# Kernel optimization log

Measured on AMD Instinct MI355X. Metric: run time of the kernel, lower is better.

Reference implementation:

```python
import jax, jax.numpy as jnp
import numpy as np

H = 128          # h_dim
N_NODES = 100000
N_EDGES = 1600000
N_GRAPHS = 256
EPS_BN = 1e-5


def setup_inputs() -> dict:
    key = jax.random.key(0)
    ks = jax.random.split(key, 12)
    x = jax.random.normal(ks[0], (N_NODES, 4), dtype=jnp.float32)
    edge_index = jax.random.randint(ks[1], (2, N_EDGES), 0, N_NODES, dtype=jnp.int64)
    batch = jnp.sort(jax.random.randint(ks[2], (N_NODES,), 0, N_GRAPHS, dtype=jnp.int64))
    # Linear weights (xavier-ish scale), stored as [in, out]
    W1 = jax.random.normal(ks[3], (4, H), dtype=jnp.float32) * (1.0 / np.sqrt(4))
    W2 = jax.random.normal(ks[4], (H, H), dtype=jnp.float32) * (1.0 / np.sqrt(H))
    W3 = jax.random.normal(ks[5], (H, H), dtype=jnp.float32) * (1.0 / np.sqrt(H))
    Wfc = jax.random.normal(ks[6], (H, 1), dtype=jnp.float32) * (1.0 / np.sqrt(H))
    def bn_params(k):
        k1, k2, k3, k4 = jax.random.split(k, 4)
        gamma = 1.0 + 0.1 * jax.random.normal(k1, (H,), dtype=jnp.float32)
        beta = 0.1 * jax.random.normal(k2, (H,), dtype=jnp.float32)
        mean = 0.1 * jax.random.normal(k3, (H,), dtype=jnp.float32)
        var = 1.0 + 0.1 * jax.random.uniform(k4, (H,), dtype=jnp.float32)
        return gamma, beta, mean, var
    g1, b1, m1, v1 = bn_params(ks[7])
    g2, b2, m2, v2 = bn_params(ks[8])
    g3, b3, m3, v3 = bn_params(ks[9])
    return {
        "x": x, "edge_index": edge_index, "batch": batch,
        "W1": W1, "g1": g1, "b1": b1, "m1": m1, "v1": v1,
        "W2": W2, "g2": g2, "b2": b2, "m2": m2, "v2": v2,
        "W3": W3, "g3": g3, "b3": b3, "m3": m3, "v3": v3,
        "Wfc": Wfc,
    }


def _gin_layer(h, src, dst, W, gamma, beta, mean, var):
    # GINConv with eps=0: mlp(x + sum_{j in N(i)} x_j)
    aggr = jax.ops.segment_sum(h[src], dst, num_segments=N_NODES)
    z = (h + aggr) @ W                                  # Linear(bias=False)
    z = (z - mean) * (gamma / jnp.sqrt(var + EPS_BN)) + beta  # BatchNorm1d (eval)
    return jax.nn.relu(z)


def reference(x, edge_index, batch,
              W1, g1, b1, m1, v1,
              W2, g2, b2, m2, v2,
              W3, g3, b3, m3, v3,
              Wfc):
    src, dst = edge_index[0], edge_index[1]
    h = _gin_layer(x, src, dst, W1, g1, b1, m1, v1)
    h = _gin_layer(h, src, dst, W2, g2, b2, m2, v2)
    h = _gin_layer(h, src, dst, W3, g3, b3, m3, v3)
    # dropout: identity in eval mode
    sums = jax.ops.segment_sum(h, batch, num_segments=N_GRAPHS)      # [G, H]
    cnts = jax.ops.segment_sum(jnp.ones((N_NODES, 1), h.dtype), batch,
                               num_segments=N_GRAPHS)                # [G, 1]
    pooled = sums / jnp.maximum(cnts, 1.0)
    return jax.nn.sigmoid(pooled @ Wfc)                               # [G, 1]
```

## Files before the change

### kernel.cpp

```cpp
#include <hip/hip_runtime.h>
#include <hip/hip_fp8.h>
#include <math.h>

#define N_NODES 100000
#define N_EDGES 1600000
#define N_GRAPHS 256
#define H 128
#define EPS_BN 1e-5f
#define ELLW 64

#define PSZ 256
#define PSH 8
#define P_PART 391
#define NB_BLD 782
#define EPT_B 8
#define EPB_B (256 * EPT_B)

typedef unsigned int uint;
typedef unsigned short ushort;
typedef __attribute__((ext_vector_type(8))) short bf16x8;
typedef __attribute__((ext_vector_type(4))) float f32x4;
typedef __attribute__((ext_vector_type(2))) float f32x2;
typedef __attribute__((ext_vector_type(4))) int i32x4;

__device__ __forceinline__ uint f2bf_bits(float x) {
    uint u = __float_as_uint(x);
    return (u + 0x7fffu + ((u >> 16) & 1u)) >> 16;
}
__device__ __forceinline__ uint pack_bf2(float a, float b) {
    return f2bf_bits(a) | (f2bf_bits(b) << 16);
}

__device__ __forceinline__ unsigned char f32_to_fp8(float x) {
#if __has_builtin(__builtin_amdgcn_cvt_pk_fp8_f32)
    int v = __builtin_amdgcn_cvt_pk_fp8_f32(x, 0.0f, 0, false);
    return (unsigned char)(v & 0xff);
#else
    __hip_fp8_e4m3 q(x);
    return (unsigned char)q.__x;
#endif
}
__device__ __forceinline__ f32x4 fp8x4_to_f32x4(uint v) {
    f32x4 r;
#if __has_builtin(__builtin_amdgcn_cvt_pk_f32_fp8)
    f32x2 lo = __builtin_amdgcn_cvt_pk_f32_fp8((int)v, false);
    f32x2 hi = __builtin_amdgcn_cvt_pk_f32_fp8((int)v, true);
    r.x = lo.x; r.y = lo.y; r.z = hi.x; r.w = hi.y;
#else
    __hip_fp8_e4m3 a, b, c, d;
    a.__x = (unsigned char)(v & 0xff);
    b.__x = (unsigned char)((v >> 8) & 0xff);
    c.__x = (unsigned char)((v >> 16) & 0xff);
    d.__x = (unsigned char)((v >> 24) & 0xff);
    r.x = (float)a; r.y = (float)b; r.z = (float)c; r.w = (float)d;
#endif
    return r;
}

__global__ __launch_bounds__(256) void k_hist(const int* __restrict__ dst,
                                              int* __restrict__ hist,
                                              const int* __restrict__ batch,
                                              int* __restrict__ gstart,
                                              const float* __restrict__ W2,
                                              ushort* __restrict__ Wpk2,
                                              const float* __restrict__ W3,
                                              ushort* __restrict__ Wpk3,
                                              float* __restrict__ Gz,
                                              uint* __restrict__ Hf8pad) {
    __shared__ int h[P_PART];
    int b = blockIdx.x;
    if (b < NB_BLD) {
        for (int i = threadIdx.x; i < P_PART; i += 256) h[i] = 0;
        __syncthreads();
        int base = b * EPB_B + threadIdx.x * EPT_B;
        #pragma unroll
        for (int j = 0; j < EPT_B / 4; j++) {
            int e = base + j * 4;
            if (e + 4 <= N_EDGES) {
                i32x4 d = __builtin_nontemporal_load((const i32x4*)&dst[e]);
                atomicAdd(&h[d.x >> PSH], 1);
                atomicAdd(&h[d.y >> PSH], 1);
                atomicAdd(&h[d.z >> PSH], 1);
                atomicAdd(&h[d.w >> PSH], 1);
            }
        }
        __syncthreads();
        for (int i = threadIdx.x; i < P_PART; i += 256)
            hist[b * P_PART + i] = h[i];
        return;
    }
    if (b < 1174) {
        int n = (b - NB_BLD) * 256 + threadIdx.x;
        if (n >= N_NODES) return;
        int g = batch[n];
        int gp = (n == 0) ? -1 : batch[n - 1];
        for (int gr = gp + 1; gr <= g; gr++) gstart[gr] = n;
        if (n == N_NODES - 1) {
            for (int gr = g + 1; gr <= N_GRAPHS; gr++) gstart[gr] = N_NODES;
        }
        return;
    }
    if (b >= 1190) {
        if (threadIdx.x < N_GRAPHS) Gz[threadIdx.x] = 0.0f;
        if (threadIdx.x < 32) Hf8pad[threadIdx.x] = 0u;
        return;
    }
    const float* W = (b < 1182) ? W2 : W3;
    ushort* Wpk = (b < 1182) ? Wpk2 : Wpk3;
    int t = ((b < 1182) ? (b - 1174) : (b - 1182)) * 256 + threadIdx.x;
    int lane = t & 63, nt = (t >> 6) & 7, kt = t >> 9;
    int n = nt * 16 + (lane & 15);
    int kbase = kt * 32 + (lane >> 4) * 8;
    ushort v[8];
    #pragma unroll
    for (int j = 0; j < 8; j++)
        v[j] = (ushort)f2bf_bits(W[(size_t)(kbase + j) * H + n]);
    uint4 pk;
    pk.x = (uint)v[0] | ((uint)v[1] << 16);
    pk.y = (uint)v[2] | ((uint)v[3] << 16);
    pk.z = (uint)v[4] | ((uint)v[5] << 16);
    pk.w = (uint)v[6] | ((uint)v[7] << 16);
    *(uint4*)&Wpk[(size_t)t * 8] = pk;
}

__global__ __launch_bounds__(256) void k_scan_a(const int* __restrict__ hist,
                                                int* __restrict__ offs,
                                                int* __restrict__ tot) {
    __shared__ int lds[256];
    int p = blockIdx.x;
    int t = threadIdx.x;
    int v0 = 0, v1 = 0, v2 = 0, v3 = 0;
    int b0 = t * 4;
    if (b0 + 0 < NB_BLD) v0 = hist[(b0 + 0) * P_PART + p];
    if (b0 + 1 < NB_BLD) v1 = hist[(b0 + 1) * P_PART + p];
    if (b0 + 2 < NB_BLD) v2 = hist[(b0 + 2) * P_PART + p];
    if (b0 + 3 < NB_BLD) v3 = hist[(b0 + 3) * P_PART + p];
    int tt = v0 + v1 + v2 + v3;
    lds[t] = tt;
    __syncthreads();
    for (int off = 1; off < 256; off <<= 1) {
        int tmp = (t >= off) ? lds[t - off] : 0;
        __syncthreads();
        lds[t] += tmp;
        __syncthreads();
    }
    int run = lds[t] - tt;
    if (b0 + 0 < NB_BLD) { offs[(b0 + 0) * P_PART + p] = run; run += v0; }
    if (b0 + 1 < NB_BLD) { offs[(b0 + 1) * P_PART + p] = run; run += v1; }
    if (b0 + 2 < NB_BLD) { offs[(b0 + 2) * P_PART + p] = run; run += v2; }
    if (b0 + 3 < NB_BLD) { offs[(b0 + 3) * P_PART + p] = run; run += v3; }
    if (t == 255) tot[p] = lds[255];
}

__global__ void k_scan_b(const int* __restrict__ tot, int* __restrict__ parr) {
    __shared__ int lds[512];
    int p = threadIdx.x;
    int v = (p < P_PART) ? tot[p] : 0;
    lds[p] = v;
    __syncthreads();
    for (int off = 1; off < 512; off <<= 1) {
        int tmp = (p >= off) ? lds[p - off] : 0;
        __syncthreads();
        lds[p] += tmp;
        __syncthreads();
    }
    if (p < P_PART) parr[p] = lds[p] - v;
    if (p == 0) parr[P_PART] = N_EDGES;
}

__global__ __launch_bounds__(256) void k_scatter(const int* __restrict__ src,
                                                 const int* __restrict__ dst,
                                                 const int* __restrict__ offs,
                                                 const int* __restrict__ parr,
                                                 uint* __restrict__ ebuf) {
    __shared__ int lofs[P_PART];
    for (int i = threadIdx.x; i < P_PART; i += 256)
        lofs[i] = offs[blockIdx.x * P_PART + i] + parr[i];
    __syncthreads();
    int base = blockIdx.x * EPB_B + threadIdx.x * EPT_B;
    #pragma unroll
    for (int j = 0; j < EPT_B / 4; j++) {
        int e = base + j * 4;
        if (e + 4 <= N_EDGES) {
            i32x4 d = __builtin_nontemporal_load((const i32x4*)&dst[e]);
            i32x4 s = __builtin_nontemporal_load((const i32x4*)&src[e]);
            #pragma unroll
            for (int k = 0; k < 4; k++) {
                int dk = (k == 0) ? d.x : (k == 1) ? d.y : (k == 2) ? d.z : d.w;
                int sk = (k == 0) ? s.x : (k == 1) ? s.y : (k == 2) ? s.z : s.w;
                int pos = atomicAdd(&lofs[dk >> PSH], 1);
                ebuf[pos] = ((uint)sk << 8) | ((uint)dk & 255u);
            }
        }
    }
}

__global__ __launch_bounds__(256) void k_build(const uint* __restrict__ ebuf,
                                               const int* __restrict__ parr,
                                               int* __restrict__ cnt,
                                               int* __restrict__ ell) {
    __shared__ int lc[PSZ];
    int p = blockIdx.x;
    for (int i = threadIdx.x; i < PSZ; i += 256) lc[i] = 0;
    __syncthreads();
    int e0 = parr[p], e1 = parr[p + 1];
    int nb = p * PSZ;
    for (int i = e0 + threadIdx.x; i < e1; i += 256) {
        uint sd = ebuf[i];
        int dl = (int)(sd & 255u);
        int slot = atomicAdd(&lc[dl], 1);
        if (slot < ELLW) ell[(size_t)(nb + dl) * ELLW + slot] = (int)(sd >> 8);
    }
    __syncthreads();
    for (int i = threadIdx.x; i < PSZ; i += 256) {
        int n = nb + i;
        if (n < N_NODES) {
            int c = lc[i];
            cnt[n] = c;
            int cc = (c < ELLW) ? c : ELLW;
            int cp = (cc + 15) & ~15;
            if (cp > ELLW) cp = ELLW;
            for (int slot = cc; slot < cp; slot++)
                ell[(size_t)n * ELLW + slot] = N_NODES;
        }
    }
}

__global__ __launch_bounds__(256) void k_layer1(
    const float* __restrict__ x, const int* __restrict__ cnt,
    const int* __restrict__ ell, const float* __restrict__ W1,
    const float* __restrict__ gamma, const float* __restrict__ beta,
    const float* __restrict__ mean, const float* __restrict__ var,
    uint* __restrict__ Hf8) {
    __shared__ float scs[128], shs[128];
    int tid = threadIdx.x;
    if (tid < 128) {
        float sc = gamma[tid] * rsqrtf(var[tid] + EPS_BN);
        scs[tid] = sc;
        shs[tid] = beta[tid] - mean[tid] * sc;
    }
    __syncthreads();
    int lane = tid & 63, wave = tid >> 6;
    int sub = lane >> 4, m = lane & 15;
    int n = blockIdx.x * 16 + wave * 4 + sub;
    if (n >= N_NODES) return;
    int cn = cnt[n]; if (cn > ELLW) cn = ELLW;
    const int* row = &ell[(size_t)n * ELLW];
    const char* xb = (const char*)x;
    float4 acc = {0.f, 0.f, 0.f, 0.f};
    for (int e = m; e < cn; e += 16) {
        float4 v = *(const float4*)(xb + ((uint)row[e] << 4));
        acc.x += v.x; acc.y += v.y; acc.z += v.z; acc.w += v.w;
    }
    #pragma unroll
    for (int off = 8; off > 0; off >>= 1) {
        acc.x += __shfl_down(acc.x, off, 16);
        acc.y += __shfl_down(acc.y, off, 16);
        acc.z += __shfl_down(acc.z, off, 16);
        acc.w += __shfl_down(acc.w, off, 16);
    }
    int src = lane & 48;
    float4 xs = *(const float4*)(xb + ((uint)n << 4));
    float uu[4];
    uu[0] = __shfl(acc.x, src, 64) + xs.x;
    uu[1] = __shfl(acc.y, src, 64) + xs.y;
    uu[2] = __shfl(acc.z, src, 64) + xs.z;
    uu[3] = __shfl(acc.w, src, 64) + xs.w;
    int j0 = m * 8;
    float z[8] = {0.f, 0.f, 0.f, 0.f, 0.f, 0.f, 0.f, 0.f};
    #pragma unroll
    for (int k = 0; k < 4; k++) {
        float4 wa = *(const float4*)&W1[k * H + j0];
        float4 wb = *(const float4*)&W1[k * H + j0 + 4];
        z[0] += uu[k] * wa.x; z[1] += uu[k] * wa.y;
        z[2] += uu[k] * wa.z; z[3] += uu[k] * wa.w;
        z[4] += uu[k] * wb.x; z[5] += uu[k] * wb.y;
        z[6] += uu[k] * wb.z; z[7] += uu[k] * wb.w;
    }
    #pragma unroll
    for (int i = 0; i < 8; i++)
        z[i] = fmaxf(z[i] * scs[j0 + i] + shs[j0 + i], 0.0f);
    uint2 q;
    q.x = (uint)f32_to_fp8(z[0]) | ((uint)f32_to_fp8(z[1]) << 8)
        | ((uint)f32_to_fp8(z[2]) << 16) | ((uint)f32_to_fp8(z[3]) << 24);
    q.y = (uint)f32_to_fp8(z[4]) | ((uint)f32_to_fp8(z[5]) << 8)
        | ((uint)f32_to_fp8(z[6]) << 16) | ((uint)f32_to_fp8(z[7]) << 24);
    *(uint2*)&Hf8[(size_t)n * 32 + m * 2] = q;
}

__global__ __launch_bounds__(256) void k_aggr128(
    const uint* __restrict__ Hf8, const int* __restrict__ cnt,
    const int* __restrict__ ell, uint* __restrict__ Ubf) {
    int t = blockIdx.x * 256 + threadIdx.x;
    int n = t >> 6, lane = t & 63;
    if (n >= N_NODES) return;
    int g = lane >> 4, c8 = lane & 15;
    const int* row = &ell[(size_t)n * ELLW];
    const char* Hb = (const char*)Hf8;
    uint co = (uint)c8 << 3;
    i32x4 id = *(const i32x4*)(row + 4 * g);
    uint2 sp = {0u, 0u};
    if (g == 0) sp = *(const uint2*)(Hb + (((uint)n << 7) | co));
    int cn = cnt[n]; if (cn > ELLW) cn = ELLW;
    int cnp = (cn + 15) & ~15; if (cnp > ELLW) cnp = ELLW;

    f32x4 A = {0.f, 0.f, 0.f, 0.f};
    f32x4 B = {0.f, 0.f, 0.f, 0.f};
    for (int e = 0; e < cnp; e += 16) {
        i32x4 idn = id;
        if (e + 16 < cnp) idn = *(const i32x4*)(row + e + 16 + 4 * g);
        uint2 p0 = *(const uint2*)(Hb + (((uint)id.x << 7) | co));
        uint2 p1 = *(const uint2*)(Hb + (((uint)id.y << 7) | co));
        uint2 p2 = *(const uint2*)(Hb + (((uint)id.z << 7) | co));
        uint2 p3 = *(const uint2*)(Hb + (((uint)id.w << 7) | co));
        f32x4 l0 = fp8x4_to_f32x4(p0.x), h0 = fp8x4_to_f32x4(p0.y);
        f32x4 l1 = fp8x4_to_f32x4(p1.x), h1 = fp8x4_to_f32x4(p1.y);
        f32x4 l2 = fp8x4_to_f32x4(p2.x), h2 = fp8x4_to_f32x4(p2.y);
        f32x4 l3 = fp8x4_to_f32x4(p3.x), h3 = fp8x4_to_f32x4(p3.y);
        A += (l0 + l1) + (l2 + l3);
        B += (h0 + h1) + (h2 + h3);
        id = idn;
    }
    if (g == 0) {
        A += fp8x4_to_f32x4(sp.x);
        B += fp8x4_to_f32x4(sp.y);
    }
    #pragma unroll
    for (int off = 32; off >= 16; off >>= 1) {
        A.x += __shfl_down(A.x, off, 64);
        A.y += __shfl_down(A.y, off, 64);
        A.z += __shfl_down(A.z, off, 64);
        A.w += __shfl_down(A.w, off, 64);
        B.x += __shfl_down(B.x, off, 64);
        B.y += __shfl_down(B.y, off, 64);
        B.z += __shfl_down(B.z, off, 64);
        B.w += __shfl_down(B.w, off, 64);
    }
    if (g == 0) {
        uint4 ov;
        ov.x = pack_bf2(A.x, A.y);
        ov.y = pack_bf2(A.z, A.w);
        ov.z = pack_bf2(B.x, B.y);
        ov.w = pack_bf2(B.z, B.w);
        *(uint4*)&Ubf[(size_t)n * 64 + c8 * 4] = ov;
    }
}

__global__ __launch_bounds__(256) void k_gemm_mfma(
    const uint* __restrict__ Ubf, const uint* __restrict__ Wpk,
    const float* __restrict__ gamma, const float* __restrict__ beta,
    const float* __restrict__ mean, const float* __restrict__ var,
    unsigned char* __restrict__ Hf8,
    const int* __restrict__ batch, const float* __restrict__ Wfc,
    float* __restrict__ Gz, int mode) {
    __shared__ uint lds_u[64 * 68];
    __shared__ float sc_s[128], sh_s[128];
    __shared__ float wfc[128];
    __shared__ int bb[64];
    __shared__ float sblk[64];
    int tid = threadIdx.x;
    int row0 = blockIdx.x * 64;
    if (tid < 128) {
        float sc = gamma[tid] * rsqrtf(var[tid] + EPS_BN);
        sc_s[tid] = sc;
        sh_s[tid] = beta[tid] - mean[tid] * sc;
    }
    if (mode == 2) {
        if (tid < 128) wfc[tid] = Wfc[tid];
        if (tid < 64) {
            int rr = row0 + tid;
            bb[tid] = (rr < N_NODES) ? batch[rr] : -1;
        }
    }
    #pragma unroll
    for (int it = 0; it < 4; it++) {
        int r = it * 16 + (tid >> 4);
        int c = (tid & 15) * 4;
        int gr = row0 + r; if (gr >= N_NODES) gr = N_NODES - 1;
        uint4 v = *(const uint4*)&Ubf[(size_t)gr * 64 + c];
        *(uint4*)&lds_u[r * 68 + c] = v;
    }
    __syncthreads();

    int wave = tid >> 6, lane = tid & 63;
    int m = lane & 15, quad = lane >> 4;
    bf16x8 a[4];
    #pragma unroll
    for (int kt = 0; kt < 4; kt++)
        a[kt] = *(const bf16x8*)&lds_u[(wave * 16 + m) * 68 + kt * 16 + quad * 4];

    f32x4 acc[8];
    #pragma unroll
    for (int nt = 0; nt < 8; nt++) acc[nt] = (f32x4){0.f, 0.f, 0.f, 0.f};

    #pragma unroll
    for (int nt = 0; nt < 8; nt++) {
        #pragma unroll
        for (int kt = 0; kt < 4; kt++) {
            bf16x8 b = *(const bf16x8*)&Wpk[((size_t)(kt * 8 + nt) * 64 + lane) * 4];
            acc[nt] = __builtin_amdgcn_mfma_f32_16x16x32_bf16(a[kt], b, acc[nt], 0, 0, 0);
        }
    }

    if (mode == 1) {
        #pragma unroll
        for (int nt = 0; nt < 8; nt++) {
            int col = nt * 16 + m;
            float sc = sc_s[col], sh = sh_s[col];
            #pragma unroll
            for (int r = 0; r < 4; r++) {
                int row = row0 + wave * 16 + quad * 4 + r;
                if (row < N_NODES) {
                    float z = fmaxf(acc[nt][r] * sc + sh, 0.0f);
                    Hf8[(size_t)row * 128 + col] = f32_to_fp8(z);
                }
            }
        }
    } else {
        float pr[4] = {0.f, 0.f, 0.f, 0.f};
        #pragma unroll
        for (int nt = 0; nt < 8; nt++) {
            int col = nt * 16 + m;
            float sc = sc_s[col], sh = sh_s[col];
            float wf = wfc[col];
            #pragma unroll
            for (int r = 0; r < 4; r++) {
                float z = fmaxf(acc[nt][r] * sc + sh, 0.0f);
                pr[r] += z * wf;
            }
        }
        #pragma unroll
        for (int r = 0; r < 4; r++) {
            float p = pr[r];
            p += __shfl_down(p, 8, 16);
            p += __shfl_down(p, 4, 16);
            p += __shfl_down(p, 2, 16);
            p += __shfl_down(p, 1, 16);
            if (m == 0) sblk[wave * 16 + quad * 4 + r] = p;
        }
        __syncthreads();
        if (tid == 0) {
            int i = 0;
            while (i < 64 && row0 + i < N_NODES) {
                int g = bb[i];
                float s = 0.0f;
                while (i < 64 && row0 + i < N_NODES && bb[i] == g) {
                    s += sblk[i]; i++;
                }
                atomicAdd(&Gz[g], s);
            }
        }
    }
}

__global__ void k_fc(const float* __restrict__ Gz, const int* __restrict__ gstart,
                     float* __restrict__ out) {
    int g = threadIdx.x;
    if (g < N_GRAPHS) {
        int c = gstart[g + 1] - gstart[g];
        float z = Gz[g] / fmaxf((float)c, 1.0f);
        out[g] = 1.0f / (1.0f + expf(-z));
    }
}

extern "C" void kernel_launch(void* const* d_in, const int* in_sizes, int n_in,
                              void* d_out, int out_size, void* d_ws, size_t ws_size,
                              hipStream_t stream) {
    const float* x     = (const float*)d_in[0];
    const int*   ei    = (const int*)d_in[1];
    const int*   batch = (const int*)d_in[2];
    const float* W1    = (const float*)d_in[3];
    const float* g1    = (const float*)d_in[4];
    const float* b1    = (const float*)d_in[5];
    const float* m1    = (const float*)d_in[6];
    const float* v1    = (const float*)d_in[7];
    const float* W2    = (const float*)d_in[8];
    const float* g2    = (const float*)d_in[9];
    const float* b2    = (const float*)d_in[10];
    const float* m2    = (const float*)d_in[11];
    const float* v2    = (const float*)d_in[12];
    const float* W3    = (const float*)d_in[13];
    const float* g3    = (const float*)d_in[14];
    const float* b3    = (const float*)d_in[15];
    const float* m3    = (const float*)d_in[16];
    const float* v3    = (const float*)d_in[17];
    const float* Wfc   = (const float*)d_in[18];
    float* out = (float*)d_out;

    const int* srcp = ei;
    const int* dstp = ei + N_EDGES;

    uint* Ubf  = (uint*)d_ws;
    uint* Hf8u = Ubf + (size_t)N_NODES * 64;
    int* cnt   = (int*)(Hf8u + (size_t)N_NODES * 32 + 32);
    int* ell   = cnt + N_NODES;
    int* gstart = ell + (size_t)N_NODES * ELLW;
    ushort* Wpk2 = (ushort*)(gstart + 260);
    ushort* Wpk3 = Wpk2 + 16384;
    int* hist  = (int*)(Wpk3 + 16384);
    int* offs  = hist + NB_BLD * P_PART;
    int* parr  = offs + NB_BLD * P_PART;
    int* tot   = parr + 400;
    float* Gz  = (float*)(tot + 400);
    uint* ebuf = Ubf;
    uint* Hf8pad = Hf8u + (size_t)N_NODES * 32;

    k_hist<<<1191, 256, 0, stream>>>(dstp, hist, batch, gstart, W2, Wpk2, W3, Wpk3,
                                     Gz, Hf8pad);
    k_scan_a<<<P_PART, 256, 0, stream>>>(hist, offs, tot);
    k_scan_b<<<1, 512, 0, stream>>>(tot, parr);
    k_scatter<<<NB_BLD, 256, 0, stream>>>(srcp, dstp, offs, parr, ebuf);
    k_build<<<P_PART, 256, 0, stream>>>(ebuf, parr, cnt, ell);

    k_layer1<<<(N_NODES + 15) / 16, 256, 0, stream>>>(
        x, cnt, ell, W1, g1, b1, m1, v1, Hf8u);
    k_aggr128<<<(N_NODES * 64 + 255) / 256, 256, 0, stream>>>(Hf8u, cnt, ell, Ubf);
    k_gemm_mfma<<<(N_NODES + 63) / 64, 256, 0, stream>>>(
        Ubf, (const uint*)Wpk2, g2, b2, m2, v2, (unsigned char*)Hf8u,
        batch, Wfc, Gz, 1);
    k_aggr128<<<(N_NODES * 64 + 255) / 256, 256, 0, stream>>>(Hf8u, cnt, ell, Ubf);
    k_gemm_mfma<<<(N_NODES + 63) / 64, 256, 0, stream>>>(
        Ubf, (const uint*)Wpk3, g3, b3, m3, v3, (unsigned char*)Hf8u,
        batch, Wfc, Gz, 2);
    k_fc<<<1, 256, 0, stream>>>(Gz, gstart, out);
}
```

Before: 271.6 us.

## Fold partition scan and final FC into neighboring kernels; coalesce fp8 stores

Removes the single-block scan kernel by having each scatter and build block recompute the partition prefix sum of tot in shared memory. Removes the final FC kernel by having the last-finishing block of the layer-3 gemm compute the mean and sigmoid, detected with an atomic counter and a fence. In layer 2, the fp8 activations are staged through shared memory and written as 16-byte row chunks instead of byte-wise stores. The cost is redundant per-block scans and an extra barrier and atomic in the gemm.

```diff
diff --git a/kernel.cpp b/kernel.cpp
--- a/kernel.cpp
+++ b/kernel.cpp
@@ -57,6 +57,27 @@
     return r;
 }
 
+__device__ __forceinline__ void scan_parr(const int* __restrict__ tot,
+                                          int* lparr, int* ltmp) {
+    int t = threadIdx.x;
+    int i0 = 2 * t, i1 = 2 * t + 1;
+    int a = (i0 < P_PART) ? tot[i0] : 0;
+    int b = (i1 < P_PART) ? tot[i1] : 0;
+    int s = a + b;
+    ltmp[t] = s;
+    __syncthreads();
+    for (int off = 1; off < 256; off <<= 1) {
+        int v = (t >= off) ? ltmp[t - off] : 0;
+        __syncthreads();
+        ltmp[t] += v;
+        __syncthreads();
+    }
+    int ex = ltmp[t] - s;
+    if (i0 < 392) lparr[i0] = ex;
+    if (i1 < 392) lparr[i1] = ex + a;
+    __syncthreads();
+}
+
 __global__ __launch_bounds__(256) void k_hist(const int* __restrict__ dst,
                                               int* __restrict__ hist,
                                               const int* __restrict__ batch,
@@ -66,7 +87,8 @@
                                               const float* __restrict__ W3,
                                               ushort* __restrict__ Wpk3,
                                               float* __restrict__ Gz,
-                                              uint* __restrict__ Hf8pad) {
+                                              uint* __restrict__ Hf8pad,
+                                              int* __restrict__ done) {
     __shared__ int h[P_PART];
     int b = blockIdx.x;
     if (b < NB_BLD) {
@@ -103,6 +125,7 @@
     if (b >= 1190) {
         if (threadIdx.x < N_GRAPHS) Gz[threadIdx.x] = 0.0f;
         if (threadIdx.x < 32) Hf8pad[threadIdx.x] = 0u;
+        if (threadIdx.x == 0) *done = 0;
         return;
     }
     const float* W = (b < 1182) ? W2 : W3;
@@ -152,30 +175,17 @@
     if (t == 255) tot[p] = lds[255];
 }
 
-__global__ void k_scan_b(const int* __restrict__ tot, int* __restrict__ parr) {
-    __shared__ int lds[512];
-    int p = threadIdx.x;
-    int v = (p < P_PART) ? tot[p] : 0;
-    lds[p] = v;
-    __syncthreads();
-    for (int off = 1; off < 512; off <<= 1) {
-        int tmp = (p >= off) ? lds[p - off] : 0;
-        __syncthreads();
-        lds[p] += tmp;
-        __syncthreads();
-    }
-    if (p < P_PART) parr[p] = lds[p] - v;
-    if (p == 0) parr[P_PART] = N_EDGES;
-}
-
 __global__ __launch_bounds__(256) void k_scatter(const int* __restrict__ src,
                                                  const int* __restrict__ dst,
                                                  const int* __restrict__ offs,
-                                                 const int* __restrict__ parr,
+                                                 const int* __restrict__ tot,
                                                  uint* __restrict__ ebuf) {
     __shared__ int lofs[P_PART];
+    __shared__ int ltmp[256];
+    __shared__ int lparr[392];
+    scan_parr(tot, lparr, ltmp);
     for (int i = threadIdx.x; i < P_PART; i += 256)
-        lofs[i] = offs[blockIdx.x * P_PART + i] + parr[i];
+        lofs[i] = offs[blockIdx.x * P_PART + i] + lparr[i];
     __syncthreads();
     int base = blockIdx.x * EPB_B + threadIdx.x * EPT_B;
     #pragma unroll
@@ -196,14 +206,17 @@
 }
 
 __global__ __launch_bounds__(256) void k_build(const uint* __restrict__ ebuf,
-                                               const int* __restrict__ parr,
+                                               const int* __restrict__ tot,
                                                int* __restrict__ cnt,
                                                int* __restrict__ ell) {
     __shared__ int lc[PSZ];
+    __shared__ int ltmp[256];
+    __shared__ int lparr[392];
+    scan_parr(tot, lparr, ltmp);
     int p = blockIdx.x;
     for (int i = threadIdx.x; i < PSZ; i += 256) lc[i] = 0;
     __syncthreads();
-    int e0 = parr[p], e1 = parr[p + 1];
+    int e0 = lparr[p], e1 = lparr[p + 1];
     int nb = p * PSZ;
     for (int i = e0 + threadIdx.x; i < e1; i += 256) {
         uint sd = ebuf[i];
@@ -352,12 +365,15 @@
     const float* __restrict__ mean, const float* __restrict__ var,
     unsigned char* __restrict__ Hf8,
     const int* __restrict__ batch, const float* __restrict__ Wfc,
-    float* __restrict__ Gz, int mode) {
+    float* __restrict__ Gz, const int* __restrict__ gstart,
+    float* __restrict__ out, int* __restrict__ done, int mode) {
     __shared__ uint lds_u[64 * 68];
     __shared__ float sc_s[128], sh_s[128];
     __shared__ float wfc[128];
     __shared__ int bb[64];
     __shared__ float sblk[64];
+    __shared__ int lastblk;
+    unsigned char* lds_o = (unsigned char*)lds_u;
     int tid = threadIdx.x;
     int row0 = blockIdx.x * 64;
     if (tid < 128) {
@@ -388,6 +404,7 @@
     #pragma unroll
     for (int kt = 0; kt < 4; kt++)
         a[kt] = *(const bf16x8*)&lds_u[(wave * 16 + m) * 68 + kt * 16 + quad * 4];
+    __syncthreads();
 
     f32x4 acc[8];
     #pragma unroll
@@ -409,12 +426,19 @@
             float sc = sc_s[col], sh = sh_s[col];
             #pragma unroll
             for (int r = 0; r < 4; r++) {
-                int row = row0 + wave * 16 + quad * 4 + r;
-                if (row < N_NODES) {
-                    float z = fmaxf(acc[nt][r] * sc + sh, 0.0f);
-                    Hf8[(size_t)row * 128 + col] = f32_to_fp8(z);
-                }
+                int rl = wave * 16 + quad * 4 + r;
+                float z = fmaxf(acc[nt][r] * sc + sh, 0.0f);
+                lds_o[rl * 128 + col] = f32_to_fp8(z);
             }
+        }
+        __syncthreads();
+        #pragma unroll
+        for (int i = tid; i < 512; i += 256) {
+            int r = i >> 3;
+            int off = (i & 7) * 16;
+            int grow = row0 + r;
+            if (grow < N_NODES)
+                *(uint4*)&Hf8[(size_t)grow * 128 + off] = *(const uint4*)&lds_o[i * 16];
         }
     } else {
         float pr[4] = {0.f, 0.f, 0.f, 0.f};
@@ -449,17 +473,16 @@
                 }
                 atomicAdd(&Gz[g], s);
             }
-        }
-    }
-}
-
-__global__ void k_fc(const float* __restrict__ Gz, const int* __restrict__ gstart,
-                     float* __restrict__ out) {
-    int g = threadIdx.x;
-    if (g < N_GRAPHS) {
-        int c = gstart[g + 1] - gstart[g];
-        float z = Gz[g] / fmaxf((float)c, 1.0f);
-        out[g] = 1.0f / (1.0f + expf(-z));
+            __threadfence();
+            int v = atomicAdd(done, 1);
+            lastblk = (v == (int)gridDim.x - 1) ? 1 : 0;
+        }
+        __syncthreads();
+        if (lastblk && tid < N_GRAPHS) {
+            int c = gstart[tid + 1] - gstart[tid];
+            float z = atomicAdd(&Gz[tid], 0.0f) / fmaxf((float)c, 1.0f);
+            out[tid] = 1.0f / (1.0f + expf(-z));
+        }
     }
 }
 
@@ -499,28 +522,26 @@
     ushort* Wpk3 = Wpk2 + 16384;
     int* hist  = (int*)(Wpk3 + 16384);
     int* offs  = hist + NB_BLD * P_PART;
-    int* parr  = offs + NB_BLD * P_PART;
-    int* tot   = parr + 400;
+    int* tot   = offs + NB_BLD * P_PART;
     float* Gz  = (float*)(tot + 400);
+    int* done  = (int*)(Gz + N_GRAPHS);
     uint* ebuf = Ubf;
     uint* Hf8pad = Hf8u + (size_t)N_NODES * 32;
 
     k_hist<<<1191, 256, 0, stream>>>(dstp, hist, batch, gstart, W2, Wpk2, W3, Wpk3,
-                                     Gz, Hf8pad);
+                                     Gz, Hf8pad, done);
     k_scan_a<<<P_PART, 256, 0, stream>>>(hist, offs, tot);
-    k_scan_b<<<1, 512, 0, stream>>>(tot, parr);
-    k_scatter<<<NB_BLD, 256, 0, stream>>>(srcp, dstp, offs, parr, ebuf);
-    k_build<<<P_PART, 256, 0, stream>>>(ebuf, parr, cnt, ell);
+    k_scatter<<<NB_BLD, 256, 0, stream>>>(srcp, dstp, offs, tot, ebuf);
+    k_build<<<P_PART, 256, 0, stream>>>(ebuf, tot, cnt, ell);
 
     k_layer1<<<(N_NODES + 15) / 16, 256, 0, stream>>>(
         x, cnt, ell, W1, g1, b1, m1, v1, Hf8u);
     k_aggr128<<<(N_NODES * 64 + 255) / 256, 256, 0, stream>>>(Hf8u, cnt, ell, Ubf);
     k_gemm_mfma<<<(N_NODES + 63) / 64, 256, 0, stream>>>(
         Ubf, (const uint*)Wpk2, g2, b2, m2, v2, (unsigned char*)Hf8u,
-        batch, Wfc, Gz, 1);
+        batch, Wfc, Gz, gstart, out, done, 1);
     k_aggr128<<<(N_NODES * 64 + 255) / 256, 256, 0, stream>>>(Hf8u, cnt, ell, Ubf);
     k_gemm_mfma<<<(N_NODES + 63) / 64, 256, 0, stream>>>(
         Ubf, (const uint*)Wpk3, g3, b3, m3, v3, (unsigned char*)Hf8u,
-        batch, Wfc, Gz, 2);
-    k_fc<<<1, 256, 0, stream>>>(Gz, gstart, out);
-}
+        batch, Wfc, Gz, gstart, out, done, 2);
+}
```

After: 300.3 us. +10.5%, slower.
